# Optimization experiments

Hardware: AMD Instinct MI355X
Metric: run time of the kernel (lower is better)

Reference implementation:

```python
import jax, jax.numpy as jnp
import numpy as np

B, L, D = 1, 4096, 2048
H, KVH, HD = 8, 2, 256
WINDOW = 512
BASE = 10000.0
ROPE_FRACTION = 1.0


def _rms_norm(x, scale=None):
    x32 = x.astype(jnp.float32)
    var = jnp.mean(jnp.square(x32), axis=-1, keepdims=True)
    xn = x32 * jax.lax.rsqrt(var + 1e-6)
    return xn if scale is None else xn * scale.astype(jnp.float32)


def _apply_rope(x, positions, base, rope_fraction):
    head_dim = x.shape[-1]
    rope_dim = int(head_dim * rope_fraction)
    if rope_dim == 0:
        return x
    half = rope_dim // 2
    head_half = head_dim // 2
    freq_exp = 2.0 * jnp.arange(half, dtype=jnp.float32) / head_dim
    timescale = base ** freq_exp
    pos = positions[..., None].astype(jnp.float32)          # [B, L, 1]
    sinusoid = pos / timescale[None, None, :]               # [B, L, half]
    sin = jnp.sin(sinusoid)[:, :, None, :]                  # [B, L, 1, half]
    cos = jnp.cos(sinusoid)[:, :, None, :]
    x1 = x[..., :half]
    x2 = x[..., head_half:head_half + half]
    x1r = x1 * cos - x2 * sin
    x2r = x2 * cos + x1 * sin
    if rope_dim == head_dim:
        return jnp.concatenate([x1r, x2r], axis=-1)
    return jnp.concatenate(
        [x1r, x[..., half:head_half], x2r, x[..., head_half + half:]], axis=-1)


def setup_inputs() -> dict:
    key = jax.random.key(0)
    ks = jax.random.split(key, 5)
    x = jax.random.normal(ks[0], (B, L, D), dtype=jnp.float32)
    positions = jnp.broadcast_to(jnp.arange(L, dtype=jnp.int32)[None, :], (B, L))
    s = 0.02
    Wq = jax.random.normal(ks[1], (D, H * HD), dtype=jnp.float32) * s
    Wk = jax.random.normal(ks[2], (D, KVH * HD), dtype=jnp.float32) * s
    Wv = jax.random.normal(ks[3], (D, KVH * HD), dtype=jnp.float32) * s
    Wo = jax.random.normal(ks[4], (H * HD, D), dtype=jnp.float32) * s
    q_scale = jnp.ones((HD,), dtype=jnp.float32)
    k_scale = jnp.ones((HD,), dtype=jnp.float32)
    return {"x": x, "positions": positions, "Wq": Wq, "Wk": Wk, "Wv": Wv,
            "Wo": Wo, "q_scale": q_scale, "k_scale": k_scale}


def reference(x, positions, Wq, Wk, Wv, Wo, q_scale, k_scale):
    # projections (no bias, no 1/sqrt(d) scaling, matching the source)
    q = (x @ Wq).reshape(B, L, H, HD)
    k = (x @ Wk).reshape(B, L, KVH, HD)
    v = (x @ Wv).reshape(B, L, KVH, HD)
    # QK RMSNorm (learned scale), V RMSNorm (no scale)
    q = _apply_rope(_rms_norm(q, q_scale), positions, BASE, ROPE_FRACTION)
    k = _apply_rope(_rms_norm(k, k_scale), positions, BASE, ROPE_FRACTION)
    v = _rms_norm(v)
    # GQA head repeat
    rep = H // KVH
    k = jnp.repeat(k, rep, axis=2)  # [B, L, H, HD]
    v = jnp.repeat(v, rep, axis=2)
    # attention scores [B, H, Lq, Lk]
    scores = jnp.einsum('bqhd,bkhd->bhqk', q, k)
    qi = jnp.arange(L)[:, None]
    kj = jnp.arange(L)[None, :]
    mask = (kj <= qi) & (kj >= qi - WINDOW + 1)  # causal & sliding window
    scores = jnp.where(mask[None, None, :, :], scores, -10000.0)
    probs = jax.nn.softmax(scores.astype(jnp.float32), axis=-1)
    out = jnp.einsum('bhqk,bkhd->bqhd', probs, v)
    return out.reshape(B, L, H * HD) @ Wo
```

## Files before the change

kernel.cpp:

```cpp
#include <hip/hip_runtime.h>
#include <hip/hip_bf16.h>
#include <math.h>
#include <stdint.h>

#define L_      4096
#define D_      2048
#define H_      8
#define KVH_    2
#define HD_     256
#define WINDOW_ 512
#define QKVW    3072

typedef __attribute__((ext_vector_type(8))) _Float16 f16x8;
typedef __attribute__((ext_vector_type(4))) _Float16 f16x4;
typedef __attribute__((ext_vector_type(4))) short s16x4;
typedef __attribute__((ext_vector_type(4))) float f32x4;

__device__ __forceinline__ short f2h(float f) {
    _Float16 h = (_Float16)f;
    return *reinterpret_cast<short*>(&h);
}
__device__ __forceinline__ float h2f(short s) {
    _Float16 h = *reinterpret_cast<_Float16*>(&s);
    return (float)h;
}

__device__ __forceinline__ void gl2lds16(const void* g, void* l) {
    __builtin_amdgcn_global_load_lds(
        (const __attribute__((address_space(1))) uint32_t*)g,
        (__attribute__((address_space(3))) uint32_t*)l, 16, 0, 0);
}

__global__ __launch_bounds__(256) void cast_f16(const float* __restrict__ X,
                                                short* __restrict__ Y, int n) {
    int idx = (blockIdx.x * 256 + threadIdx.x) * 8;
    if (idx >= n) return;
    float4 a = *(const float4*)(X + idx);
    float4 b = *(const float4*)(X + idx + 4);
    s16x4 o0, o1;
    o0[0]=f2h(a.x); o0[1]=f2h(a.y); o0[2]=f2h(a.z); o0[3]=f2h(a.w);
    o1[0]=f2h(b.x); o1[1]=f2h(b.y); o1[2]=f2h(b.z); o1[3]=f2h(b.w);
    *(s16x4*)(Y + idx)     = o0;
    *(s16x4*)(Y + idx + 4) = o1;
}

__global__ __launch_bounds__(256) void transpose_cast(const float* __restrict__ W,
                                                      short* __restrict__ Wt,
                                                      int K, int N) {
    __shared__ float tl[32][33];
    int t = threadIdx.x;
    int c = t & 31, r4 = (t >> 5) * 4;
    int k0 = blockIdx.y * 32, n0 = blockIdx.x * 32;
#pragma unroll
    for (int i = 0; i < 4; ++i)
        tl[r4 + i][c] = W[(size_t)(k0 + r4 + i) * N + n0 + c];
    __syncthreads();
#pragma unroll
    for (int i = 0; i < 4; ++i)
        Wt[(size_t)(n0 + r4 + i) * K + k0 + c] = f2h(tl[c][r4 + i]);
}

template <int OUT_HALF>
__global__ __launch_bounds__(256) void gemm_mfma(const short* __restrict__ A,
                                                 const short* __restrict__ Bt,
                                                 void* __restrict__ Cout,
                                                 int M, int N, int K) {
    __shared__ short As[128][64];
    __shared__ short Bs[128][64];

    const int tid = threadIdx.x;
    const int w = tid >> 6, lane = tid & 63;
    const int lq = lane & 15, quad = lane >> 4;
    const int bm = blockIdx.y * 128, bn = blockIdx.x * 128;
    const int wm = (w & 1) * 64, wn = (w >> 1) * 64;
    const int lrow = lane >> 3;
    const int slot = lane & 7;

    f32x4 acc[4][4];
#pragma unroll
    for (int i = 0; i < 4; ++i)
#pragma unroll
        for (int j = 0; j < 4; ++j) acc[i][j] = 0;

    for (int k0 = 0; k0 < K; k0 += 64) {
#pragma unroll
        for (int c = 0; c < 4; ++c) {
            const int r0 = w * 32 + c * 8;
            const int row = r0 + lrow;
            const int chunk = slot ^ (row & 7);
            gl2lds16(A  + (size_t)(bm + row) * K + k0 + chunk * 8, &As[r0][0]);
            gl2lds16(Bt + (size_t)(bn + row) * K + k0 + chunk * 8, &Bs[r0][0]);
        }
        __syncthreads();

#pragma unroll
        for (int f = 0; f < 2; ++f) {
            const int sA = (((f * 4) + quad) ^ (lq & 7)) * 8;
            f16x8 af[4], bfr[4];
#pragma unroll
            for (int i = 0; i < 4; ++i) af[i]  = *(const f16x8*)&As[wm + i * 16 + lq][sA];
#pragma unroll
            for (int j = 0; j < 4; ++j) bfr[j] = *(const f16x8*)&Bs[wn + j * 16 + lq][sA];
#pragma unroll
            for (int i = 0; i < 4; ++i)
#pragma unroll
                for (int j = 0; j < 4; ++j)
                    acc[i][j] = __builtin_amdgcn_mfma_f32_16x16x32_f16(af[i], bfr[j], acc[i][j], 0, 0, 0);
        }
        __syncthreads();
    }

#pragma unroll
    for (int i = 0; i < 4; ++i)
#pragma unroll
        for (int r = 0; r < 4; ++r) {
            int row = bm + wm + i * 16 + quad * 4 + r;
#pragma unroll
            for (int j = 0; j < 4; ++j) {
                int col = bn + wn + j * 16 + lq;
                float v = acc[i][j][r];
                if (OUT_HALF) ((short*)Cout)[(size_t)row * N + col] = f2h(v);
                else          ((float*)Cout)[(size_t)row * N + col] = v;
            }
        }
}

__global__ __launch_bounds__(256) void norm_rope_w(short* __restrict__ qkv,
                                                   const float* __restrict__ q_scale,
                                                   const float* __restrict__ k_scale,
                                                   const int* __restrict__ positions) {
    const int w = threadIdx.x >> 6, lane = threadIdx.x & 63;
    const int row = blockIdx.x * 4 + w;
    const int token = row / 12, ridx = row % 12;
    short* p = qkv + (size_t)token * QKVW + ridx * HD_ + lane * 4;

    const s16x4 raw = *(const s16x4*)p;
    float xv[4];
#pragma unroll
    for (int i = 0; i < 4; ++i) xv[i] = h2f(raw[i]);
    float ss = xv[0]*xv[0] + xv[1]*xv[1] + xv[2]*xv[2] + xv[3]*xv[3];
#pragma unroll
    for (int off = 32; off > 0; off >>= 1) ss += __shfl_xor(ss, off);
    const float rinv = rsqrtf(ss * (1.0f / (float)HD_) + 1e-6f);
#pragma unroll
    for (int i = 0; i < 4; ++i) xv[i] *= rinv;

    if (ridx < 10) {
        const float* scp = (ridx < 8 ? q_scale : k_scale) + lane * 4;
        const float4 sc = *(const float4*)scp;
        xv[0] *= sc.x; xv[1] *= sc.y; xv[2] *= sc.z; xv[3] *= sc.w;

        const int pos = positions[token];
        float ov[4];
#pragma unroll
        for (int i = 0; i < 4; ++i) ov[i] = __shfl_xor(xv[i], 32);
        const float sgn = (lane < 32) ? -1.0f : 1.0f;
        const int dbase = (lane & 31) * 4;
#pragma unroll
        for (int i = 0; i < 4; ++i) {
            const float fe = (float)(dbase + i) * (1.0f / 128.0f);
            const float inv_ts = __expf(fe * -9.210340371976184f);
            const float ang = (float)pos * inv_ts;
            float s, c;
            __sincosf(ang, &s, &c);
            xv[i] = xv[i] * c + sgn * ov[i] * s;
        }
    }

    s16x4 o;
#pragma unroll
    for (int i = 0; i < 4; ++i) o[i] = f2h(xv[i]);
    *(s16x4*)p = o;
}

__global__ __launch_bounds__(256) void vt_prep(const short* __restrict__ qkv,
                                               short* __restrict__ vtg) {
    const int tok0 = blockIdx.x * 64;
    const int g = blockIdx.y;
    const int tid = threadIdx.x;
    __shared__ short Vs[64][264];
#pragma unroll
    for (int i = 0; i < 8; ++i) {
        int f = (tid + i * 256) * 8;
        int tok = f >> 8, d = f & 255;
        *(int4*)&Vs[tok][d] =
            *(const int4*)(qkv + (size_t)(tok0 + tok) * QKVW + 2560 + g * HD_ + d);
    }
    __syncthreads();
    const int d = tid;
    short tmp[64];
#pragma unroll
    for (int j = 0; j < 64; ++j) tmp[j] = Vs[j][d];
    short* dst = vtg + ((size_t)g * HD_ + d) * L_ + tok0;
#pragma unroll
    for (int c = 0; c < 8; ++c)
        *(int4*)(dst + c * 8) = *(const int4*)&tmp[c * 8];
}

__global__ __launch_bounds__(256) void attn_mfma(const short* __restrict__ qkv,
                                                 const short* __restrict__ vtg,
                                                 short* __restrict__ ao) {
    const int bx = blockIdx.x;
    const int g = bx & 1, qt = bx >> 1;
    const int q0 = qt * 16;
    const int tid = threadIdx.x;
    const int w = tid >> 6, lane = tid & 63;
    const int lq = lane & 15, quad = lane >> 4;
    const int h = g * 4 + w;

    __shared__ short lds[18688];
    short (*Ks)[264] = (short (*)[264])lds;
    short (*Vt)[40]  = (short (*)[40])(lds + 8448);

    f16x8 qf[8];
    {
        const short* qrow = qkv + (size_t)(q0 + lq) * QKVW + h * HD_;
#pragma unroll
        for (int f = 0; f < 8; ++f)
            qf[f] = *(const f16x8*)(qrow + f * 32 + quad * 8);
    }

    float m_run = -INFINITY, l_run = 0.0f;

    f32x4 accO[16];
#pragma unroll
    for (int dt = 0; dt < 16; ++dt) accO[dt] = 0;

    const short* kcol = qkv + 2048 + g * HD_;
    const short* vrow = vtg + (size_t)g * HD_ * L_;
    const int qi = q0 + lq;

    for (int kt = 0; kt < 17; ++kt) {
        const int kbase = q0 - WINDOW_ + kt * 32;
        if (kbase + 32 <= 0) continue;

        {
            const int row = tid >> 3;
            const int co = (tid & 7) * 32;
            int kj = kbase + row;
            kj = min(max(kj, 0), L_ - 1);
            const short* src = kcol + (size_t)kj * QKVW + co;
            short* dst = &Ks[row][co];
#pragma unroll
            for (int u = 0; u < 4; ++u)
                *(int4*)(dst + u * 8) = *(const int4*)(src + u * 8);
        }
        {
            const short* src = vrow + (size_t)tid * L_;
#pragma unroll
            for (int c = 0; c < 4; ++c) {
                int ck = kbase + c * 8;
                ck = min(max(ck, 0), L_ - 8);
                *(int4*)&Vt[tid][c * 8] = *(const int4*)(src + ck);
            }
        }
        __syncthreads();

        f32x4 st0 = 0, st1 = 0;
#pragma unroll
        for (int f = 0; f < 8; ++f) {
            f16x8 kf0 = *(const f16x8*)&Ks[lq][f * 32 + quad * 8];
            f16x8 kf1 = *(const f16x8*)&Ks[16 + lq][f * 32 + quad * 8];
            st0 = __builtin_amdgcn_mfma_f32_16x16x32_f16(kf0, qf[f], st0, 0, 0, 0);
            st1 = __builtin_amdgcn_mfma_f32_16x16x32_f16(kf1, qf[f], st1, 0, 0, 0);
        }

        const int kA = kbase + quad * 4;
        const int kB = kA + 16;
        float sv[8]; bool vd[8];
#pragma unroll
        for (int r = 0; r < 4; ++r) {
            int ka = kA + r, kb = kB + r;
            vd[r]     = (ka >= 0) && (ka <= qi) && (ka > qi - WINDOW_);
            vd[4 + r] = (kb >= 0) && (kb <= qi) && (kb > qi - WINDOW_);
            sv[r]     = vd[r]     ? st0[r] : -INFINITY;
            sv[4 + r] = vd[4 + r] ? st1[r] : -INFINITY;
        }
        float mt = sv[0];
#pragma unroll
        for (int i = 1; i < 8; ++i) mt = fmaxf(mt, sv[i]);
        mt = fmaxf(mt, __shfl_xor(mt, 16));
        mt = fmaxf(mt, __shfl_xor(mt, 32));
        const float mn = fmaxf(m_run, mt);
        const float alpha = (mn == -INFINITY) ? 1.0f : __expf(m_run - mn);
        float pv[8], rs = 0.0f;
#pragma unroll
        for (int i = 0; i < 8; ++i) {
            pv[i] = vd[i] ? __expf(sv[i] - mn) : 0.0f;
            rs += pv[i];
        }
        rs += __shfl_xor(rs, 16);
        rs += __shfl_xor(rs, 32);
        m_run = mn;
        l_run = l_run * alpha + rs;

        f16x4 p0, p1;
#pragma unroll
        for (int i = 0; i < 4; ++i) { p0[i] = (_Float16)pv[i]; p1[i] = (_Float16)pv[4 + i]; }

#pragma unroll
        for (int dt = 0; dt < 16; ++dt) {
            f16x4 v0 = *(const f16x4*)&Vt[dt * 16 + lq][quad * 4];
            f16x4 v1 = *(const f16x4*)&Vt[dt * 16 + lq][16 + quad * 4];
            f32x4 t = accO[dt];
#pragma unroll
            for (int r = 0; r < 4; ++r) t[r] *= alpha;
            t = __builtin_amdgcn_mfma_f32_16x16x16f16(v0, p0, t, 0, 0, 0);
            t = __builtin_amdgcn_mfma_f32_16x16x16f16(v1, p1, t, 0, 0, 0);
            accO[dt] = t;
        }
        __syncthreads();
    }

    const float inv = 1.0f / l_run;
    short* myE = lds + w * 4224;
#pragma unroll
    for (int dt = 0; dt < 16; ++dt) {
        f16x4 e;
#pragma unroll
        for (int r = 0; r < 4; ++r) e[r] = (_Float16)(accO[dt][r] * inv);
        *(f16x4*)&myE[lq * 264 + dt * 16 + quad * 4] = e;
    }
    {
        const int row = lane >> 2;
        const int c0 = (lane & 3) * 64;
        short* orow = ao + (size_t)(q0 + row) * 2048 + h * HD_ + c0;
#pragma unroll
        for (int u = 0; u < 8; ++u)
            *(int4*)(orow + u * 8) = *(const int4*)&myE[row * 264 + c0 + u * 8];
    }
}

extern "C" void kernel_launch(void* const* d_in, const int* in_sizes, int n_in,
                              void* d_out, int out_size, void* d_ws, size_t ws_size,
                              hipStream_t stream) {
    const float* x         = (const float*)d_in[0];
    const int*   positions = (const int*)d_in[1];
    const float* Wq        = (const float*)d_in[2];
    const float* Wk        = (const float*)d_in[3];
    const float* Wv        = (const float*)d_in[4];
    const float* Wo        = (const float*)d_in[5];
    const float* q_scale   = (const float*)d_in[6];
    const float* k_scale   = (const float*)d_in[7];
    float*       out       = (float*)d_out;

    char* ws = (char*)d_ws;
    short* xb    = (short*)(ws);
    short* qkv   = (short*)(ws + 16777216);
    short* ao    = (short*)(ws + 41943040);
    short* Wtqkv = (short*)(ws + 58720256);
    short* Wto   = (short*)(ws + 71303168);
    short* vtg   = xb;

    cast_f16<<<4096, 256, 0, stream>>>(x, xb, L_ * D_);
    transpose_cast<<<dim3(2048 / 32, 2048 / 32), 256, 0, stream>>>(Wq, Wtqkv, D_, 2048);
    transpose_cast<<<dim3(512 / 32, 2048 / 32), 256, 0, stream>>>(Wk, Wtqkv + (size_t)2048 * D_, D_, 512);
    transpose_cast<<<dim3(512 / 32, 2048 / 32), 256, 0, stream>>>(Wv, Wtqkv + (size_t)2560 * D_, D_, 512);
    transpose_cast<<<dim3(2048 / 32, 2048 / 32), 256, 0, stream>>>(Wo, Wto, 2048, 2048);

    gemm_mfma<1><<<dim3(QKVW / 128, L_ / 128), 256, 0, stream>>>(xb, Wtqkv, qkv, L_, QKVW, D_);

    norm_rope_w<<<(L_ * 12) / 4, 256, 0, stream>>>(qkv, q_scale, k_scale, positions);

    vt_prep<<<dim3(L_ / 64, KVH_), 256, 0, stream>>>(qkv, vtg);

    attn_mfma<<<(L_ / 16) * KVH_, 256, 0, stream>>>(qkv, vtg, ao);

    gemm_mfma<0><<<dim3(D_ / 128, L_ / 128), 256, 0, stream>>>(ao, Wto, out, L_, D_, 2048);
}
```

Before: 319.8 us.

## Double-buffer K/V tiles with direct global-to-LDS loads in attention kernel

The attention loop now stages the next K/V tile into a second LDS buffer with direct global-to-LDS loads while the current tile is computed, using explicit vmcnt waits and raw barriers in place of syncthreads. LDS layouts are XOR-swizzled so the MFMA operand reads avoid bank conflicts, and leading fully-masked tiles are skipped by computing the starting tile. s_setprio raises wave priority around the MFMA sections. The aim is to hide global load latency behind compute, at the cost of more LDS per block, which may reduce occupancy, and reliance on hand-counted vmcnt values being correct.

Result: faster. 301.0 us (-5.9%).

```diff
diff --git a/kernel.cpp b/kernel.cpp
--- a/kernel.cpp
+++ b/kernel.cpp
@@ -208,9 +208,7 @@
     const int lq = lane & 15, quad = lane >> 4;
     const int h = g * 4 + w;
 
-    __shared__ short lds[18688];
-    short (*Ks)[264] = (short (*)[264])lds;
-    short (*Vt)[40]  = (short (*)[40])(lds + 8448);
+    __shared__ short lds[32768];
 
     f16x8 qf[8];
     {
@@ -230,49 +228,67 @@
     const short* vrow = vtg + (size_t)g * HD_ * L_;
     const int qi = q0 + lq;
 
-    for (int kt = 0; kt < 17; ++kt) {
+    const int kl5 = lane >> 5;
+    const int ksl = lane & 31;
+    const int vdm = ((lane >> 5) << 3) | (lane & 7);
+    const int vkc = (lane >> 3) & 3;
+
+    auto stageKV = [&](int b, int kb) {
+#pragma unroll
+        for (int i = 0; i < 4; ++i) {
+            const int r0 = w * 8 + 2 * i;
+            const int row = r0 + kl5;
+            const int cs = ksl ^ (row & 7);
+            const int kj = min(max(kb + row, 0), L_ - 1);
+            gl2lds16(kcol + (size_t)kj * QKVW + cs * 8, lds + b * 8192 + r0 * 256);
+        }
+        const int ck = min(max(kb + vkc * 8, 0), L_ - 8);
+#pragma unroll
+        for (int j = 0; j < 4; ++j) {
+            const int wv = w * 4 + j;
+            gl2lds16(vrow + (size_t)(wv * 16 + vdm) * L_ + ck,
+                     lds + 16384 + b * 8192 + wv * 512);
+        }
+    };
+
+    const int kt0 = (q0 >= 480) ? 0 : ((480 - q0) / 32 + 1);
+    int buf = 0;
+    stageKV(0, q0 - WINDOW_ + kt0 * 32);
+
+    for (int kt = kt0; kt < 17; ++kt) {
         const int kbase = q0 - WINDOW_ + kt * 32;
-        if (kbase + 32 <= 0) continue;
-
-        {
-            const int row = tid >> 3;
-            const int co = (tid & 7) * 32;
-            int kj = kbase + row;
-            kj = min(max(kj, 0), L_ - 1);
-            const short* src = kcol + (size_t)kj * QKVW + co;
-            short* dst = &Ks[row][co];
-#pragma unroll
-            for (int u = 0; u < 4; ++u)
-                *(int4*)(dst + u * 8) = *(const int4*)(src + u * 8);
-        }
-        {
-            const short* src = vrow + (size_t)tid * L_;
-#pragma unroll
-            for (int c = 0; c < 4; ++c) {
-                int ck = kbase + c * 8;
-                ck = min(max(ck, 0), L_ - 8);
-                *(int4*)&Vt[tid][c * 8] = *(const int4*)(src + ck);
-            }
-        }
-        __syncthreads();
+        if (kt < 16) {
+            stageKV(buf ^ 1, kbase + 32);
+            asm volatile("s_waitcnt vmcnt(8)" ::: "memory");
+        } else {
+            asm volatile("s_waitcnt vmcnt(0)" ::: "memory");
+        }
+        __builtin_amdgcn_s_barrier();
+        __builtin_amdgcn_sched_barrier(0);
+
+        const short* KsB = lds + buf * 8192;
+        const short* VtB = lds + 16384 + buf * 8192;
 
         f32x4 st0 = 0, st1 = 0;
+        __builtin_amdgcn_s_setprio(1);
 #pragma unroll
         for (int f = 0; f < 8; ++f) {
-            f16x8 kf0 = *(const f16x8*)&Ks[lq][f * 32 + quad * 8];
-            f16x8 kf1 = *(const f16x8*)&Ks[16 + lq][f * 32 + quad * 8];
+            const int sl = ((f * 4 + quad) ^ (lq & 7)) * 8;
+            f16x8 kf0 = *(const f16x8*)(KsB + lq * 256 + sl);
+            f16x8 kf1 = *(const f16x8*)(KsB + (16 + lq) * 256 + sl);
             st0 = __builtin_amdgcn_mfma_f32_16x16x32_f16(kf0, qf[f], st0, 0, 0, 0);
             st1 = __builtin_amdgcn_mfma_f32_16x16x32_f16(kf1, qf[f], st1, 0, 0, 0);
         }
+        __builtin_amdgcn_s_setprio(0);
 
         const int kA = kbase + quad * 4;
         const int kB = kA + 16;
         float sv[8]; bool vd[8];
 #pragma unroll
         for (int r = 0; r < 4; ++r) {
-            int ka = kA + r, kb = kB + r;
+            int ka = kA + r, kb2 = kB + r;
             vd[r]     = (ka >= 0) && (ka <= qi) && (ka > qi - WINDOW_);
-            vd[4 + r] = (kb >= 0) && (kb <= qi) && (kb > qi - WINDOW_);
+            vd[4 + r] = (kb2 >= 0) && (kb2 <= qi) && (kb2 > qi - WINDOW_);
             sv[r]     = vd[r]     ? st0[r] : -INFINITY;
             sv[4 + r] = vd[4 + r] ? st1[r] : -INFINITY;
         }
@@ -298,10 +314,13 @@
 #pragma unroll
         for (int i = 0; i < 4; ++i) { p0[i] = (_Float16)pv[i]; p1[i] = (_Float16)pv[4 + i]; }
 
+        const int sl0 = ((lq >> 3) << 5) | ((quad >> 1) << 3) | (lq & 7);
+        const int hh = (quad & 1) * 4;
+        __builtin_amdgcn_s_setprio(1);
 #pragma unroll
         for (int dt = 0; dt < 16; ++dt) {
-            f16x4 v0 = *(const f16x4*)&Vt[dt * 16 + lq][quad * 4];
-            f16x4 v1 = *(const f16x4*)&Vt[dt * 16 + lq][16 + quad * 4];
+            f16x4 v0 = *(const f16x4*)(VtB + dt * 512 + sl0 * 8 + hh);
+            f16x4 v1 = *(const f16x4*)(VtB + dt * 512 + (sl0 | 16) * 8 + hh);
             f32x4 t = accO[dt];
 #pragma unroll
             for (int r = 0; r < 4; ++r) t[r] *= alpha;
@@ -309,7 +328,11 @@
             t = __builtin_amdgcn_mfma_f32_16x16x16f16(v1, p1, t, 0, 0, 0);
             accO[dt] = t;
         }
-        __syncthreads();
+        __builtin_amdgcn_s_setprio(0);
+
+        __builtin_amdgcn_s_barrier();
+        __builtin_amdgcn_sched_barrier(0);
+        buf ^= 1;
     }
 
     const float inv = 1.0f / l_run;
```
